# Performance work log

Measured on AMD Instinct MI355X. Metric: run time of the kernel, lower is better.

Reference implementation:

```python
import jax, jax.numpy as jnp
import numpy as np

N_NODES = 100000
N_EDGES = 1600000
N_GRAPHS = 64
HID = 128
N_EXPERTS = 8
IN_DIM = 4


def setup_inputs() -> dict:
    key = jax.random.key(0)
    ks = jax.random.split(key, 12)
    atomic_numbers = jax.random.uniform(ks[0], (N_NODES,), dtype=jnp.float32) * 80.0
    pos = jax.random.normal(ks[1], (N_NODES, 3), dtype=jnp.float32)
    edge_index = jax.random.randint(ks[2], (2, N_EDGES), 0, N_NODES, dtype=jnp.int64)
    batch = jnp.sort(jax.random.randint(ks[3], (N_NODES,), 0, N_GRAPHS, dtype=jnp.int64))
    s1 = 1.0 / np.sqrt(IN_DIM)
    s2 = 1.0 / np.sqrt(HID)
    W1 = jax.random.uniform(ks[4], (IN_DIM, HID), jnp.float32, -s1, s1)
    b1 = jnp.zeros((HID,), jnp.float32)
    W2 = jax.random.uniform(ks[5], (HID, HID), jnp.float32, -s2, s2)
    b2 = jnp.zeros((HID,), jnp.float32)
    Wlin = jax.random.uniform(ks[6], (HID, N_EXPERTS), jnp.float32, -s2, s2)
    blin = jax.random.uniform(ks[7], (N_EXPERTS,), jnp.float32, -s2, s2)
    return {"atomic_numbers": atomic_numbers, "pos": pos, "edge_index": edge_index,
            "batch": batch, "W1": W1, "b1": b1, "W2": W2, "b2": b2,
            "Wlin": Wlin, "blin": blin}


def _gcn_conv(x, W, b, src, dst, deg_inv_sqrt, n_nodes):
    # PyG GCNConv: x' = W x; aggregate deg^-1/2[src]*deg^-1/2[dst] * x'[src] into dst; + bias
    h = x @ W  # [N, out]
    norm = deg_inv_sqrt[src] * deg_inv_sqrt[dst]  # [E+N]
    msg = h[src] * norm[:, None]  # gathered, normalized messages
    out = jax.ops.segment_sum(msg, dst, num_segments=n_nodes)
    return out + b


def reference(atomic_numbers, pos, edge_index, batch, W1, b1, W2, b2, Wlin, blin):
    n = atomic_numbers.shape[0]
    x = jnp.concatenate([atomic_numbers[:, None], pos], axis=-1)  # [N, 4]
    # add self-loops (GCNConv default add_self_loops=True)
    loop = jnp.arange(n, dtype=edge_index.dtype)
    src = jnp.concatenate([edge_index[0], loop])
    dst = jnp.concatenate([edge_index[1], loop])
    deg = jax.ops.segment_sum(jnp.ones_like(dst, dtype=jnp.float32), dst, num_segments=n)
    deg_inv_sqrt = jnp.where(deg > 0, jax.lax.rsqrt(jnp.maximum(deg, 1e-12)), 0.0)
    x = _gcn_conv(x, W1, b1, src, dst, deg_inv_sqrt, n)
    x = jax.nn.relu(x)
    # dropout p=0.5 is identity in eval mode
    x = _gcn_conv(x, W2, b2, src, dst, deg_inv_sqrt, n)
    x = x @ Wlin + blin  # [N, num_experts]
    # global_mean_pool over graph ids
    sums = jax.ops.segment_sum(x, batch, num_segments=N_GRAPHS)
    cnts = jax.ops.segment_sum(jnp.ones((n,), jnp.float32), batch, num_segments=N_GRAPHS)
    pooled = sums / jnp.maximum(cnts, 1.0)[:, None]
    return jax.nn.log_softmax(pooled, axis=1)
```

## Files before the change

kernel.cpp:

```cpp
#include <hip/hip_runtime.h>
#include <math.h>

#define HID 128
#define NEXP 8
#define NGRAPH 64
#define EPC 2048
#define MAXB 512
#define NXC 8
#define NREP 8
#define NPS 8

__device__ inline unsigned short f2bf(float f) {
    unsigned u = __float_as_uint(f);
    u += 0x7FFF + ((u >> 16) & 1);
    return (unsigned short)(u >> 16);
}
__device__ inline unsigned packbf(float lo, float hi) {
    return (unsigned)f2bf(lo) | ((unsigned)f2bf(hi) << 16);
}
__device__ inline float bflo(unsigned u) { return __uint_as_float(u << 16); }
__device__ inline float bfhi(unsigned u) { return __uint_as_float(u & 0xFFFF0000u); }

__global__ void k_init0(float* __restrict__ pool, float* __restrict__ pcnt,
                        const float* __restrict__ W2, const float* __restrict__ Wlin,
                        const float* __restrict__ b2, float* __restrict__ C,
                        float* __restrict__ bb2, int* __restrict__ gcur8,
                        int mregions, int capx) {
    int i = blockIdx.x * 256 + threadIdx.x;
    if (i < mregions) gcur8[i] = i * capx;
    if (i < NREP * NGRAPH * NEXP) pool[i] = 0.0f;
    if (i < NREP * NGRAPH) pcnt[i] = 0.0f;
    int ci = i - NREP * NGRAPH * NEXP;
    if (ci >= 0 && ci < HID * NEXP) {
        int k = ci >> 3, j = ci & 7;
        float s = 0.0f;
        for (int m = 0; m < HID; m++) s += W2[k * HID + m] * Wlin[m * NEXP + j];
        C[ci] = s;
    }
    int bi = ci - HID * NEXP;
    if (bi >= 0 && bi < NEXP) {
        float s = 0.0f;
        for (int m = 0; m < HID; m++) s += b2[m] * Wlin[m * NEXP + bi];
        bb2[bi] = s;
    }
}

__global__ void __launch_bounds__(256) k_binA(
        const int* __restrict__ src, const int* __restrict__ dst,
        int* __restrict__ gcur8, unsigned* __restrict__ binned, int e, int nbuck) {
    __shared__ int h[MAXB];
    __shared__ int lstart[MAXB];
    __shared__ int lcur[MAXB];
    __shared__ int gbase[MAXB];
    __shared__ int wtot[4];
    __shared__ unsigned packed[EPC];
    __shared__ unsigned short sbkt[EPC];
    int c = blockIdx.x, t = threadIdx.x;
    int w = t >> 6, lane = t & 63;
    int x = c & (NXC - 1);
    int start = c * EPC;
    int m = e - start < EPC ? e - start : EPC;

    int d[8], sv[8];
#pragma unroll
    for (int j = 0; j < 8; j++) {
        int idx = j * 256 + t;
        if (idx < m) { d[j] = dst[start + idx]; sv[j] = src[start + idx]; }
    }
    h[t] = 0; h[t + 256] = 0;
    __syncthreads();
#pragma unroll
    for (int j = 0; j < 8; j++)
        if (j * 256 + t < m) atomicAdd(&h[d[j] >> 8], 1);
    __syncthreads();
    int v0 = h[2 * t], v1 = h[2 * t + 1];
    int sum = v0 + v1;
    int incl = sum;
#pragma unroll
    for (int dd = 1; dd < 64; dd <<= 1) {
        int y = __shfl_up(incl, dd, 64);
        if (lane >= dd) incl += y;
    }
    if (lane == 63) wtot[w] = incl;
    __syncthreads();
    int pre = 0;
#pragma unroll
    for (int ww = 0; ww < 4; ww++) pre += (ww < w) ? wtot[ww] : 0;
    int ex = pre + incl - sum;
    lstart[2 * t] = ex;     lstart[2 * t + 1] = ex + v0;
    lcur[2 * t]   = ex;     lcur[2 * t + 1]   = ex + v0;
    for (int b = t; b < nbuck; b += 256)
        gbase[b] = h[b] ? atomicAdd(&gcur8[b * NXC + x], h[b]) : 0;
    __syncthreads();
#pragma unroll
    for (int j = 0; j < 8; j++) {
        if (j * 256 + t < m) {
            int b = d[j] >> 8;
            int p = atomicAdd(&lcur[b], 1);
            packed[p] = ((unsigned)(d[j] & 255) << 24) | (unsigned)sv[j];
            sbkt[p] = (unsigned short)b;
        }
    }
    __syncthreads();
    for (int idx = t; idx < m; idx += 256) {
        int b = sbkt[idx];
        binned[gbase[b] + (idx - lstart[b])] = packed[idx];
    }
}

__global__ void k_binB(const unsigned* __restrict__ binned, const int* __restrict__ gcur8,
                       const float* __restrict__ an, const float* __restrict__ pos,
                       int* __restrict__ cnt, int* __restrict__ off,
                       float* __restrict__ dinv, float4* __restrict__ xs,
                       int* __restrict__ eidx, int n, int capx) {
    __shared__ int h[256];
    __shared__ int cur[256];
    __shared__ int wtot[4];
    int b = blockIdx.x, t = threadIdx.x;
    int w = t >> 6, lane = t & 63;
    int cbase = b * NXC;
    int ob = cbase * capx;
    h[t] = 0;
    __syncthreads();
#pragma unroll
    for (int x = 0; x < NXC; x++) {
        int rs = (cbase + x) * capx, re = gcur8[cbase + x];
        for (int k = rs + t; k < re; k += 256)
            atomicAdd(&h[binned[k] >> 24], 1);
    }
    __syncthreads();
    int v = h[t];
    int incl = v;
#pragma unroll
    for (int dd = 1; dd < 64; dd <<= 1) {
        int y = __shfl_up(incl, dd, 64);
        if (lane >= dd) incl += y;
    }
    if (lane == 63) wtot[w] = incl;
    __syncthreads();
    int pre = 0;
#pragma unroll
    for (int ww = 0; ww < 4; ww++) pre += (ww < w) ? wtot[ww] : 0;
    int ex = pre + incl - v;
    cur[t] = ex;
    int node = (b << 8) + t;
    if (node < n) {
        float di = rsqrtf((float)v + 1.0f);
        cnt[node]  = v;
        off[node]  = ob + ex;
        dinv[node] = di;
        xs[node] = make_float4(an[node] * di, pos[3 * node] * di,
                               pos[3 * node + 1] * di, pos[3 * node + 2] * di);
    }
    __syncthreads();
#pragma unroll
    for (int x = 0; x < NXC; x++) {
        int rs = (cbase + x) * capx, re = gcur8[cbase + x];
        for (int k = rs + t; k < re; k += 256) {
            unsigned u = binned[k];
            int p = atomicAdd(&cur[u >> 24], 1);
            eidx[ob + p] = (int)(u & 0xFFFFFF);
        }
    }
}

__global__ void k_gxz(const float4* __restrict__ xs, const int* __restrict__ eidx,
                      const int* __restrict__ off, const int* __restrict__ cnt,
                      const float* __restrict__ dinv, const float* __restrict__ W1,
                      const float* __restrict__ b1, const float* __restrict__ C,
                      uint4* __restrict__ z, int n) {
    int i = blockIdx.x * 256 + threadIdx.x;
    if (i >= n) return;
    float4 a = xs[i];
    int o = off[i], c = cnt[i];
    int k = 0;
    for (; k + 8 <= c; k += 8) {
        int id[8];
#pragma unroll
        for (int j = 0; j < 8; j++) id[j] = eidx[o + k + j];
        float4 vv[8];
#pragma unroll
        for (int j = 0; j < 8; j++) vv[j] = xs[id[j]];
#pragma unroll
        for (int j = 0; j < 8; j++) {
            a.x += vv[j].x; a.y += vv[j].y; a.z += vv[j].z; a.w += vv[j].w;
        }
    }
    for (; k < c; k++) {
        float4 vv = xs[eidx[o + k]];
        a.x += vv.x; a.y += vv.y; a.z += vv.z; a.w += vv.w;
    }
    float di = dinv[i];
    float z0 = 0.f, z1 = 0.f, z2 = 0.f, z3 = 0.f,
          z4 = 0.f, z5 = 0.f, z6 = 0.f, z7 = 0.f;
#pragma unroll 4
    for (int kk = 0; kk < HID; kk++) {
        float x1k = fmaxf(di * (a.x * W1[kk] + a.y * W1[HID + kk] +
                                a.z * W1[2 * HID + kk] + a.w * W1[3 * HID + kk])
                          + b1[kk], 0.0f);
        const float* cr = C + kk * NEXP;
        z0 += x1k * cr[0]; z1 += x1k * cr[1];
        z2 += x1k * cr[2]; z3 += x1k * cr[3];
        z4 += x1k * cr[4]; z5 += x1k * cr[5];
        z6 += x1k * cr[6]; z7 += x1k * cr[7];
    }
    uint4 outv;
    outv.x = packbf(z0 * di, z1 * di);
    outv.y = packbf(z2 * di, z3 * di);
    outv.z = packbf(z4 * di, z5 * di);
    outv.w = packbf(z6 * di, z7 * di);
    z[i] = outv;
}

__global__ void k_gz(const uint4* __restrict__ z4, const int* __restrict__ eidx,
                     const int* __restrict__ off, const int* __restrict__ cnt,
                     const float* __restrict__ dinv, const int* __restrict__ batch,
                     float* __restrict__ pool, float* __restrict__ pcnt, int n) {
    int t = threadIdx.x;
    int slot = t >> 4;
    int l = t & 15;
    int i0 = blockIdx.x * (16 * NPS) + slot * NPS;
    if (i0 >= n) return;
    int i1 = i0 + NPS < n ? i0 + NPS : n;
    int rep = (blockIdx.x + slot) & (NREP - 1);
    float* rp  = pool + (size_t)rep * NGRAPH * NEXP;
    float* rpc = pcnt + (size_t)rep * NGRAPH;

    int curg = -1;
    float r = 0.0f, runlen = 0.0f;
    int j = l & 7;
    for (int i = i0; i < i1; i++) {
        float a0 = 0.f, a1 = 0.f, a2 = 0.f, a3 = 0.f,
              a4 = 0.f, a5 = 0.f, a6 = 0.f, a7 = 0.f;
        int o = off[i], c = cnt[i];
        for (int k = l; k < c; k += 16) {
            uint4 zr = z4[eidx[o + k]];
            a0 += bflo(zr.x); a1 += bfhi(zr.x);
            a2 += bflo(zr.y); a3 += bfhi(zr.y);
            a4 += bflo(zr.z); a5 += bfhi(zr.z);
            a6 += bflo(zr.w); a7 += bfhi(zr.w);
        }
        if (l == 0) {
            uint4 zr = z4[i];
            a0 += bflo(zr.x); a1 += bfhi(zr.x);
            a2 += bflo(zr.y); a3 += bfhi(zr.y);
            a4 += bflo(zr.z); a5 += bfhi(zr.z);
            a6 += bflo(zr.w); a7 += bfhi(zr.w);
        }
#pragma unroll
        for (int m = 1; m < 16; m <<= 1) {
            a0 += __shfl_xor(a0, m, 64); a1 += __shfl_xor(a1, m, 64);
            a2 += __shfl_xor(a2, m, 64); a3 += __shfl_xor(a3, m, 64);
            a4 += __shfl_xor(a4, m, 64); a5 += __shfl_xor(a5, m, 64);
            a6 += __shfl_xor(a6, m, 64); a7 += __shfl_xor(a7, m, 64);
        }
        float aj;
        switch (j) {
            case 0: aj = a0; break; case 1: aj = a1; break;
            case 2: aj = a2; break; case 3: aj = a3; break;
            case 4: aj = a4; break; case 5: aj = a5; break;
            case 6: aj = a6; break; default: aj = a7; break;
        }
        float v = dinv[i] * aj;
        int g = batch[i];
        if (g != curg) {
            if (curg >= 0 && l < 8) {
                atomicAdd(&rp[curg * NEXP + j], r);
                if (l == 0) atomicAdd(&rpc[curg], runlen);
            }
            curg = g; r = v; runlen = 1.0f;
        } else { r += v; runlen += 1.0f; }
    }
    if (curg >= 0 && l < 8) {
        atomicAdd(&rp[curg * NEXP + j], r);
        if (l == 0) atomicAdd(&rpc[curg], runlen);
    }
}

__global__ void k_lsm(const float* __restrict__ pool, const float* __restrict__ pcnt,
                      const float* __restrict__ blin, const float* __restrict__ bb2,
                      float* __restrict__ out) {
    int g = threadIdx.x;
    if (g >= NGRAPH) return;
    float p[NEXP];
#pragma unroll
    for (int k = 0; k < NEXP; k++) p[k] = 0.0f;
    float cg = 0.0f;
#pragma unroll
    for (int rr = 0; rr < NREP; rr++) {
#pragma unroll
        for (int k = 0; k < NEXP; k++) p[k] += pool[rr * NGRAPH * NEXP + g * NEXP + k];
        cg += pcnt[rr * NGRAPH + g];
    }
    float inv = 1.0f / fmaxf(cg, 1.0f);
    float v[NEXP], m = -1e30f;
#pragma unroll
    for (int k = 0; k < NEXP; k++) {
        v[k] = p[k] * inv + blin[k] + bb2[k];
        m = fmaxf(m, v[k]);
    }
    float s = 0.0f;
#pragma unroll
    for (int k = 0; k < NEXP; k++) s += expf(v[k] - m);
    float ls = logf(s);
#pragma unroll
    for (int k = 0; k < NEXP; k++) out[g * NEXP + k] = v[k] - m - ls;
}

extern "C" void kernel_launch(void* const* d_in, const int* in_sizes, int n_in,
                              void* d_out, int out_size, void* d_ws, size_t ws_size,
                              hipStream_t stream) {
    const float* an   = (const float*)d_in[0];
    const float* pos  = (const float*)d_in[1];
    const int*   ei   = (const int*)d_in[2];
    const int*   batch= (const int*)d_in[3];
    const float* W1   = (const float*)d_in[4];
    const float* b1   = (const float*)d_in[5];
    const float* W2   = (const float*)d_in[6];
    const float* b2   = (const float*)d_in[7];
    const float* Wlin = (const float*)d_in[8];
    const float* blin = (const float*)d_in[9];
    float* out = (float*)d_out;

    const int n = in_sizes[0];
    const int e = in_sizes[2] / 2;
    const int* src = ei;
    const int* dst = ei + e;

    const int nbuck = (n + 255) >> 8;
    const int ch    = (e + EPC - 1) / EPC;
    const int mreg  = nbuck * NXC;
    const int capx  = 2 * (e / (mreg > 0 ? mreg : 1)) + 256;

    char* p = (char*)d_ws;
    float4* xs    = (float4*)p;       p += sizeof(float4) * (size_t)n;
    uint4*  z     = (uint4*)p;        p += sizeof(uint4) * (size_t)n;
    float* C      = (float*)p;        p += sizeof(float) * HID * NEXP;
    float* bb2    = (float*)p;        p += sizeof(float) * NEXP;
    float* dinv   = (float*)p;        p += sizeof(float) * (size_t)n;
    float* pool   = (float*)p;        p += sizeof(float) * NREP * NGRAPH * NEXP;
    float* pcnt   = (float*)p;        p += sizeof(float) * NREP * NGRAPH;
    int*   cnt    = (int*)p;          p += sizeof(int) * (size_t)n;
    int*   off    = (int*)p;          p += sizeof(int) * (size_t)n;
    int*   gcur8  = (int*)p;          p += sizeof(int) * (mreg + 8);
    unsigned* binned = (unsigned*)p;  p += sizeof(unsigned) * (size_t)mreg * capx;
    int*   eidx   = (int*)p;          p += sizeof(int) * (size_t)mreg * capx;

    const int initN = NREP * NGRAPH * NEXP + HID * NEXP + NEXP;
    const int initG = initN > mreg ? initN : mreg;
    k_init0<<<(initG + 255) / 256, 256, 0, stream>>>(pool, pcnt, W2, Wlin, b2, C,
                                                     bb2, gcur8, mreg, capx);
    k_binA<<<ch, 256, 0, stream>>>(src, dst, gcur8, binned, e, nbuck);
    k_binB<<<nbuck, 256, 0, stream>>>(binned, gcur8, an, pos, cnt, off, dinv,
                                      xs, eidx, n, capx);

    k_gxz<<<(n + 255) / 256, 256, 0, stream>>>(xs, eidx, off, cnt, dinv, W1, b1, C, z, n);

    k_gz<<<(n + 16 * NPS - 1) / (16 * NPS), 256, 0, stream>>>(z, eidx, off, cnt, dinv,
                                                              batch, pool, pcnt, n);
    k_lsm<<<1, 64, 0, stream>>>(pool, pcnt, blin, bb2, out);
}
```

Baseline: 199.0 us.

## Split histograms, vectorize edge loads, use two threads per node, cheaper shuffle reduction

k_binA now loads src/dst with int4 vector loads in a contiguous per-thread layout and splits the shared-memory histogram into two copies (one per half-block of waves) to reduce LDS atomic contention. k_gxz assigns two threads per node, each gathering alternating neighbors before combining with a shuffle, which doubles parallelism for the gather of x features. k_gz replaces the full 4-step butterfly on all 8 accumulators with a partial reduction that then selects pairs, cutting shuffle count, and issues two atomics per lane group. The cost is that k_gxz duplicates the 128-step dense MLP compute in both threads of each pair.

```diff
diff --git a/kernel.cpp b/kernel.cpp
--- a/kernel.cpp
+++ b/kernel.cpp
@@ -48,7 +48,8 @@
 __global__ void __launch_bounds__(256) k_binA(
         const int* __restrict__ src, const int* __restrict__ dst,
         int* __restrict__ gcur8, unsigned* __restrict__ binned, int e, int nbuck) {
-    __shared__ int h[MAXB];
+    __shared__ int h0[MAXB];
+    __shared__ int h1[MAXB];
     __shared__ int lstart[MAXB];
     __shared__ int lcur[MAXB];
     __shared__ int gbase[MAXB];
@@ -62,18 +63,32 @@
     int m = e - start < EPC ? e - start : EPC;
 
     int d[8], sv[8];
-#pragma unroll
-    for (int j = 0; j < 8; j++) {
-        int idx = j * 256 + t;
-        if (idx < m) { d[j] = dst[start + idx]; sv[j] = src[start + idx]; }
-    }
-    h[t] = 0; h[t + 256] = 0;
+    if (m == EPC) {
+        int4 da = ((const int4*)(dst + start))[2 * t];
+        int4 db = ((const int4*)(dst + start))[2 * t + 1];
+        int4 sa = ((const int4*)(src + start))[2 * t];
+        int4 sb = ((const int4*)(src + start))[2 * t + 1];
+        d[0] = da.x; d[1] = da.y; d[2] = da.z; d[3] = da.w;
+        d[4] = db.x; d[5] = db.y; d[6] = db.z; d[7] = db.w;
+        sv[0] = sa.x; sv[1] = sa.y; sv[2] = sa.z; sv[3] = sa.w;
+        sv[4] = sb.x; sv[5] = sb.y; sv[6] = sb.z; sv[7] = sb.w;
+    } else {
+#pragma unroll
+        for (int j = 0; j < 8; j++) {
+            int idx = t * 8 + j;
+            if (idx < m) { d[j] = dst[start + idx]; sv[j] = src[start + idx]; }
+        }
+    }
+    int* hm = (w < 2) ? h0 : h1;
+    h0[t] = 0; h0[t + 256] = 0;
+    h1[t] = 0; h1[t + 256] = 0;
     __syncthreads();
 #pragma unroll
     for (int j = 0; j < 8; j++)
-        if (j * 256 + t < m) atomicAdd(&h[d[j] >> 8], 1);
-    __syncthreads();
-    int v0 = h[2 * t], v1 = h[2 * t + 1];
+        if (t * 8 + j < m) atomicAdd(&hm[d[j] >> 8], 1);
+    __syncthreads();
+    int v0 = h0[2 * t] + h1[2 * t];
+    int v1 = h0[2 * t + 1] + h1[2 * t + 1];
     int sum = v0 + v1;
     int incl = sum;
 #pragma unroll
@@ -89,12 +104,14 @@
     int ex = pre + incl - sum;
     lstart[2 * t] = ex;     lstart[2 * t + 1] = ex + v0;
     lcur[2 * t]   = ex;     lcur[2 * t + 1]   = ex + v0;
-    for (int b = t; b < nbuck; b += 256)
-        gbase[b] = h[b] ? atomicAdd(&gcur8[b * NXC + x], h[b]) : 0;
+    for (int b = t; b < nbuck; b += 256) {
+        int hv = h0[b] + h1[b];
+        gbase[b] = hv ? atomicAdd(&gcur8[b * NXC + x], hv) : 0;
+    }
     __syncthreads();
 #pragma unroll
     for (int j = 0; j < 8; j++) {
-        if (j * 256 + t < m) {
+        if (t * 8 + j < m) {
             int b = d[j] >> 8;
             int p = atomicAdd(&lcur[b], 1);
             packed[p] = ((unsigned)(d[j] & 255) << 24) | (unsigned)sv[j];
@@ -169,27 +186,30 @@
                       const float* __restrict__ dinv, const float* __restrict__ W1,
                       const float* __restrict__ b1, const float* __restrict__ C,
                       uint4* __restrict__ z, int n) {
-    int i = blockIdx.x * 256 + threadIdx.x;
+    int tid = blockIdx.x * 256 + threadIdx.x;
+    int i = tid >> 1;
+    int par = tid & 1;
     if (i >= n) return;
-    float4 a = xs[i];
+    float4 a = par ? make_float4(0.f, 0.f, 0.f, 0.f) : xs[i];
     int o = off[i], c = cnt[i];
-    int k = 0;
-    for (; k + 8 <= c; k += 8) {
-        int id[8];
-#pragma unroll
-        for (int j = 0; j < 8; j++) id[j] = eidx[o + k + j];
-        float4 vv[8];
-#pragma unroll
-        for (int j = 0; j < 8; j++) vv[j] = xs[id[j]];
-#pragma unroll
-        for (int j = 0; j < 8; j++) {
-            a.x += vv[j].x; a.y += vv[j].y; a.z += vv[j].z; a.w += vv[j].w;
-        }
-    }
-    for (; k < c; k++) {
-        float4 vv = xs[eidx[o + k]];
-        a.x += vv.x; a.y += vv.y; a.z += vv.z; a.w += vv.w;
-    }
+    int k = par;
+    for (; k + 6 < c; k += 8) {
+        int i0 = eidx[o + k],     i1 = eidx[o + k + 2];
+        int i2 = eidx[o + k + 4], i3 = eidx[o + k + 6];
+        float4 v0 = xs[i0], v1 = xs[i1], v2 = xs[i2], v3 = xs[i3];
+        a.x += v0.x + v1.x + v2.x + v3.x;
+        a.y += v0.y + v1.y + v2.y + v3.y;
+        a.z += v0.z + v1.z + v2.z + v3.z;
+        a.w += v0.w + v1.w + v2.w + v3.w;
+    }
+    for (; k < c; k += 2) {
+        float4 v0 = xs[eidx[o + k]];
+        a.x += v0.x; a.y += v0.y; a.z += v0.z; a.w += v0.w;
+    }
+    a.x += __shfl_xor(a.x, 1, 64);
+    a.y += __shfl_xor(a.y, 1, 64);
+    a.z += __shfl_xor(a.z, 1, 64);
+    a.w += __shfl_xor(a.w, 1, 64);
     float di = dinv[i];
     float z0 = 0.f, z1 = 0.f, z2 = 0.f, z3 = 0.f,
           z4 = 0.f, z5 = 0.f, z6 = 0.f, z7 = 0.f;
@@ -204,12 +224,14 @@
         z4 += x1k * cr[4]; z5 += x1k * cr[5];
         z6 += x1k * cr[6]; z7 += x1k * cr[7];
     }
-    uint4 outv;
-    outv.x = packbf(z0 * di, z1 * di);
-    outv.y = packbf(z2 * di, z3 * di);
-    outv.z = packbf(z4 * di, z5 * di);
-    outv.w = packbf(z6 * di, z7 * di);
-    z[i] = outv;
+    if (par == 0) {
+        uint4 outv;
+        outv.x = packbf(z0 * di, z1 * di);
+        outv.y = packbf(z2 * di, z3 * di);
+        outv.z = packbf(z4 * di, z5 * di);
+        outv.w = packbf(z6 * di, z7 * di);
+        z[i] = outv;
+    }
 }
 
 __global__ void k_gz(const uint4* __restrict__ z4, const int* __restrict__ eidx,
@@ -225,10 +247,10 @@
     int rep = (blockIdx.x + slot) & (NREP - 1);
     float* rp  = pool + (size_t)rep * NGRAPH * NEXP;
     float* rpc = pcnt + (size_t)rep * NGRAPH;
+    int Q = l >> 2;
 
     int curg = -1;
-    float r = 0.0f, runlen = 0.0f;
-    int j = l & 7;
+    float r0 = 0.0f, r1 = 0.0f, runlen = 0.0f;
     for (int i = i0; i < i1; i++) {
         float a0 = 0.f, a1 = 0.f, a2 = 0.f, a3 = 0.f,
               a4 = 0.f, a5 = 0.f, a6 = 0.f, a7 = 0.f;
@@ -247,32 +269,38 @@
             a4 += bflo(zr.z); a5 += bfhi(zr.z);
             a6 += bflo(zr.w); a7 += bfhi(zr.w);
         }
-#pragma unroll
-        for (int m = 1; m < 16; m <<= 1) {
-            a0 += __shfl_xor(a0, m, 64); a1 += __shfl_xor(a1, m, 64);
-            a2 += __shfl_xor(a2, m, 64); a3 += __shfl_xor(a3, m, 64);
-            a4 += __shfl_xor(a4, m, 64); a5 += __shfl_xor(a5, m, 64);
-            a6 += __shfl_xor(a6, m, 64); a7 += __shfl_xor(a7, m, 64);
-        }
-        float aj;
-        switch (j) {
-            case 0: aj = a0; break; case 1: aj = a1; break;
-            case 2: aj = a2; break; case 3: aj = a3; break;
-            case 4: aj = a4; break; case 5: aj = a5; break;
-            case 6: aj = a6; break; default: aj = a7; break;
-        }
-        float v = dinv[i] * aj;
+        a0 += __shfl_xor(a0, 8, 64); a1 += __shfl_xor(a1, 8, 64);
+        a2 += __shfl_xor(a2, 8, 64); a3 += __shfl_xor(a3, 8, 64);
+        a4 += __shfl_xor(a4, 8, 64); a5 += __shfl_xor(a5, 8, 64);
+        a6 += __shfl_xor(a6, 8, 64); a7 += __shfl_xor(a7, 8, 64);
+        a0 += __shfl_xor(a0, 4, 64); a1 += __shfl_xor(a1, 4, 64);
+        a2 += __shfl_xor(a2, 4, 64); a3 += __shfl_xor(a3, 4, 64);
+        a4 += __shfl_xor(a4, 4, 64); a5 += __shfl_xor(a5, 4, 64);
+        a6 += __shfl_xor(a6, 4, 64); a7 += __shfl_xor(a7, 4, 64);
+        float r0v, r1v;
+        switch (Q) {
+            case 0:  r0v = a0; r1v = a1; break;
+            case 1:  r0v = a2; r1v = a3; break;
+            case 2:  r0v = a4; r1v = a5; break;
+            default: r0v = a6; r1v = a7; break;
+        }
+        r0v += __shfl_xor(r0v, 1, 64); r1v += __shfl_xor(r1v, 1, 64);
+        r0v += __shfl_xor(r0v, 2, 64); r1v += __shfl_xor(r1v, 2, 64);
+        float di = dinv[i];
+        float v0 = di * r0v, v1 = di * r1v;
         int g = batch[i];
         if (g != curg) {
-            if (curg >= 0 && l < 8) {
-                atomicAdd(&rp[curg * NEXP + j], r);
+            if (curg >= 0 && (l & 3) == 0) {
+                atomicAdd(&rp[curg * NEXP + 2 * Q], r0);
+                atomicAdd(&rp[curg * NEXP + 2 * Q + 1], r1);
                 if (l == 0) atomicAdd(&rpc[curg], runlen);
             }
-            curg = g; r = v; runlen = 1.0f;
-        } else { r += v; runlen += 1.0f; }
-    }
-    if (curg >= 0 && l < 8) {
-        atomicAdd(&rp[curg * NEXP + j], r);
+            curg = g; r0 = v0; r1 = v1; runlen = 1.0f;
+        } else { r0 += v0; r1 += v1; runlen += 1.0f; }
+    }
+    if (curg >= 0 && (l & 3) == 0) {
+        atomicAdd(&rp[curg * NEXP + 2 * Q], r0);
+        atomicAdd(&rp[curg * NEXP + 2 * Q + 1], r1);
         if (l == 0) atomicAdd(&rpc[curg], runlen);
     }
 }
@@ -354,7 +382,8 @@
     k_binB<<<nbuck, 256, 0, stream>>>(binned, gcur8, an, pos, cnt, off, dinv,
                                       xs, eidx, n, capx);
 
-    k_gxz<<<(n + 255) / 256, 256, 0, stream>>>(xs, eidx, off, cnt, dinv, W1, b1, C, z, n);
+    k_gxz<<<(2 * n + 255) / 256, 256, 0, stream>>>(xs, eidx, off, cnt, dinv,
+                                                   W1, b1, C, z, n);
 
     k_gz<<<(n + 16 * NPS - 1) / (16 * NPS), 256, 0, stream>>>(z, eidx, off, cnt, dinv,
                                                               batch, pool, pcnt, n);
```

Measured after the change: 196.9 us. Within noise of the previous version (-1.1%).
